# Performance work log

Hardware: AMD Instinct MI355X
Metric: run time of the kernel (lower is better)

Reference implementation:

```python
import jax, jax.numpy as jnp
import numpy as np

N = 100000   # nodes
E = 1200000  # edges
D = 64       # dim == num_features
L = 5        # num_gc_layers
G = 128      # num graphs in batch
BN_EPS = 1e-5
NORM_EPS = 1e-12

def setup_inputs() -> dict:
    key = jax.random.key(0)
    ks = jax.random.split(key, 16)
    s = 0.05
    x = jax.random.normal(ks[0], (N, D), jnp.float32)
    edge_index = jax.random.randint(ks[1], (2, E), 0, N, dtype=jnp.int32)
    batch = jnp.sort(jax.random.randint(ks[2], (N,), 0, G, dtype=jnp.int32))
    # Encoder_support: Linear(D, D)
    Ws = jax.random.normal(ks[3], (D, D), jnp.float32) * s
    bs = jnp.zeros((D,), jnp.float32)
    # GIN MLPs per layer: Linear(D,D) -> ReLU -> Linear(D,D)
    W1 = jax.random.normal(ks[4], (L, D, D), jnp.float32) * s
    b1 = jnp.zeros((L, D), jnp.float32)
    W2 = jax.random.normal(ks[5], (L, D, D), jnp.float32) * s
    b2 = jnp.zeros((L, D), jnp.float32)
    # BatchNorm affine params
    bn_gamma = jnp.ones((L, D), jnp.float32)
    bn_beta = jnp.zeros((L, D), jnp.float32)
    # proj_head: Linear(L*D, L*D) -> ReLU -> Linear(L*D, L*D)
    Wp1 = jax.random.normal(ks[6], (L * D, L * D), jnp.float32) * s
    bp1 = jnp.zeros((L * D,), jnp.float32)
    Wp2 = jax.random.normal(ks[7], (L * D, L * D), jnp.float32) * s
    bp2 = jnp.zeros((L * D,), jnp.float32)
    return {"x": x, "edge_index": edge_index, "batch": batch,
            "Ws": Ws, "bs": bs, "W1": W1, "b1": b1, "W2": W2, "b2": b2,
            "bn_gamma": bn_gamma, "bn_beta": bn_beta,
            "Wp1": Wp1, "bp1": bp1, "Wp2": Wp2, "bp2": bp2}

def _l2norm(v):
    # F.normalize(v, dim=1): v / max(||v||_2, 1e-12)
    n = jnp.sqrt(jnp.sum(v * v, axis=1, keepdims=True))
    return v / jnp.maximum(n, NORM_EPS)

def reference(x, edge_index, batch, Ws, bs, W1, b1, W2, b2,
              bn_gamma, bn_beta, Wp1, bp1, Wp2, bp2):
    src, dst = edge_index[0], edge_index[1]
    h = x @ Ws + bs  # Encoder_support
    xs = []
    for i in range(L):
        # GINConv (eps=0): nn(x + sum_{j->i} x_j)
        agg = jax.ops.segment_sum(h[src], dst, num_segments=N)  # [N, D]
        z = h + agg
        z = jnp.maximum(z @ W1[i] + b1[i], 0.0) @ W2[i] + b2[i]
        z = jnp.maximum(z, 0.0)  # F.relu after conv
        # BatchNorm1d (training-mode batch stats over nodes)
        mean = jnp.mean(z, axis=0)
        var = jnp.var(z, axis=0)
        h = bn_gamma[i] * (z - mean) * jax.lax.rsqrt(var + BN_EPS) + bn_beta[i]
        xs.append(h)
    # global_add_pool per layer, concat along feature dim -> [G, L*D]
    pooled = jnp.concatenate(
        [jax.ops.segment_sum(h_, batch, num_segments=G) for h_ in xs], axis=1)
    y = jnp.maximum(pooled @ Wp1 + bp1, 0.0) @ Wp2 + bp2
    return (_l2norm(y), _l2norm(pooled))
```

## Files before the change

kernel.cpp:

```cpp
#include <hip/hip_runtime.h>
#include <hip/hip_bf16.h>
#include <hip/hip_fp16.h>

constexpr int Nn = 100000;
constexpr int Ee = 1200000;
constexpr int Ll = 5;
constexpr int Gg = 128;
constexpr int PDim = 320;

constexpr int NB    = 98;
constexpr int BCAP  = 16384;
constexpr int CHUNK = 4096;
constexpr int NBLK_A = (Ee + CHUNK - 1) / CHUNK;

typedef short short8 __attribute__((ext_vector_type(8)));
typedef float f32x4 __attribute__((ext_vector_type(4)));

union U4S8 { uint4 u; short8 s; };

__device__ inline ushort f2bf(float f) {
    const uint u = __float_as_uint(f);
    return (ushort)((u + 0x7fffu + ((u >> 16) & 1u)) >> 16);
}
__device__ inline uint pack2(float lo, float hi) {
    return (uint)f2bf(lo) | ((uint)f2bf(hi) << 16);
}
__device__ inline ushort f2h(float f) {
    const __half h = __float2half(f);
    return *(const ushort*)&h;
}
__device__ inline uint pack2h(float lo, float hi) {
    return (uint)f2h(lo) | ((uint)f2h(hi) << 16);
}
__device__ inline float h2f_lo(uint u) {
    const ushort s = (ushort)(u & 0xffffu);
    return __half2float(*(const __half*)&s);
}
__device__ inline float h2f_hi(uint u) {
    const ushort s = (ushort)(u >> 16);
    return __half2float(*(const __half*)&s);
}
__device__ inline void split2(float x0, float x1, uint& hi, uint& lo) {
    const ushort h0 = f2bf(x0), h1 = f2bf(x1);
    hi = (uint)h0 | ((uint)h1 << 16);
    const float r0 = x0 - __uint_as_float((uint)h0 << 16);
    const float r1 = x1 - __uint_as_float((uint)h1 << 16);
    lo = pack2(r0, r1);
}

__device__ inline int lower_bound_i(const int* __restrict__ a, int n, int v)
{
    int lo = 0, hi = n;
    while (lo < hi) {
        const int m = (lo + hi) >> 1;
        if (a[m] < v) lo = m + 1; else hi = m;
    }
    return lo;
}

__global__ void init_csr(const int* __restrict__ batch, int* __restrict__ gCursor,
                         int* __restrict__ cnt, float* __restrict__ sc)
{
    const int t = threadIdx.x;
    if (t < NB) gCursor[t] = t * BCAP;
    {
        const int lo = lower_bound_i(batch, Nn, t);
        const int hi = lower_bound_i(batch, Nn, t + 1);
        cnt[t] = hi - lo;
    }
    if (t < 64) { sc[t] = 1.f; sc[64 + t] = 0.f; }
}

__global__ __launch_bounds__(256) void conv_weights(
    const float* __restrict__ Ws, const float* __restrict__ W1,
    const float* __restrict__ W2, ushort* __restrict__ WThi,
    ushort* __restrict__ WTlo)
{
    const int m = blockIdx.x;
    const float* src = (m == 0) ? Ws
                     : (m <= 5) ? W1 + (size_t)(m - 1) * 4096
                                : W2 + (size_t)(m - 6) * 4096;
    ushort* dh = WThi + (size_t)m * 4096;
    ushort* dl = WTlo + (size_t)m * 4096;
    const int t = threadIdx.x;
    const int col = t & 63;
    const int k0 = (t >> 6) * 16;
    #pragma unroll
    for (int i = 0; i < 16; i++) {
        const int k = k0 + i;
        const float w = src[k * 64 + col];
        const ushort h = f2bf(w);
        dh[col * 64 + k] = h;
        dl[col * 64 + k] = f2bf(w - __uint_as_float((uint)h << 16));
    }
}

__global__ __launch_bounds__(256) void gemm_enc(
    const float* __restrict__ A1,
    const ushort* __restrict__ WThi, const ushort* __restrict__ WTlo,
    const float* __restrict__ bias, ushort* __restrict__ Ys)
{
    const int t = threadIdx.x;
    const int w = t >> 6;
    const int l = t & 63;
    const int lr = l & 15;
    const int lk = l >> 4;

    short8 bHi[4][2], bLo[4][2];
    #pragma unroll
    for (int nt = 0; nt < 4; nt++)
        #pragma unroll
        for (int c = 0; c < 2; c++) {
            const int off = (nt * 16 + lr) * 64 + c * 32 + lk * 8;
            U4S8 uh, ul;
            uh.u = *(const uint4*)(WThi + off);
            ul.u = *(const uint4*)(WTlo + off);
            bHi[nt][c] = uh.s;
            bLo[nt][c] = ul.s;
        }

    const int arow = blockIdx.x * 64 + w * 16 + lr;
    short8 aHi[2], aLo[2];
    if (arow < Nn) {
        #pragma unroll
        for (int c = 0; c < 2; c++) {
            const float* p1 = A1 + (size_t)arow * 64 + c * 32 + lk * 8;
            const float4 v0 = *(const float4*)p1;
            const float4 v1 = *(const float4*)(p1 + 4);
            U4S8 rh, rl;
            uint* ph = (uint*)&rh.u;
            uint* pl = (uint*)&rl.u;
            split2(v0.x, v0.y, ph[0], pl[0]);
            split2(v0.z, v0.w, ph[1], pl[1]);
            split2(v1.x, v1.y, ph[2], pl[2]);
            split2(v1.z, v1.w, ph[3], pl[3]);
            aHi[c] = rh.s;
            aLo[c] = rl.s;
        }
    } else {
        U4S8 z; z.u = make_uint4(0, 0, 0, 0);
        aHi[0] = aHi[1] = z.s;
        aLo[0] = aLo[1] = z.s;
    }

    f32x4 acc[4] = {};
    #pragma unroll
    for (int nt = 0; nt < 4; nt++)
        #pragma unroll
        for (int c = 0; c < 2; c++) {
            acc[nt] = __builtin_amdgcn_mfma_f32_16x16x32_bf16(
                aLo[c], bHi[nt][c], acc[nt], 0, 0, 0);
            acc[nt] = __builtin_amdgcn_mfma_f32_16x16x32_bf16(
                aHi[c], bLo[nt][c], acc[nt], 0, 0, 0);
            acc[nt] = __builtin_amdgcn_mfma_f32_16x16x32_bf16(
                aHi[c], bHi[nt][c], acc[nt], 0, 0, 0);
        }

    #pragma unroll
    for (int nt = 0; nt < 4; nt++) {
        const int ccol = nt * 16 + lr;
        const float bb = bias[ccol];
        #pragma unroll
        for (int j = 0; j < 4; j++) {
            const int crow = blockIdx.x * 64 + w * 16 + lk * 4 + j;
            if (crow < Nn)
                Ys[(size_t)crow * 64 + ccol] = f2h(acc[nt][j] + bb);
        }
    }
}

__global__ __launch_bounds__(256) void fused_mlp(
    const ushort* __restrict__ Us,
    const ushort* __restrict__ WT1hi, const ushort* __restrict__ WT1lo,
    const float* __restrict__ b1v,
    const ushort* __restrict__ WT2hi, const ushort* __restrict__ WT2lo,
    const float* __restrict__ b2v,
    ushort* __restrict__ Zs, float* __restrict__ stats)
{
    const int t = threadIdx.x;
    const int w = t >> 6;
    const int l = t & 63;
    const int lr = l & 15;
    const int lk = l >> 4;

    __shared__ ushort Mh[64][72];
    __shared__ float red[2][4][4][16];

    short8 b1Hi[4][2], b1Lo[4][2];
    #pragma unroll
    for (int nt = 0; nt < 4; nt++)
        #pragma unroll
        for (int c = 0; c < 2; c++) {
            const int off = (nt * 16 + lr) * 64 + c * 32 + lk * 8;
            U4S8 uh, ul;
            uh.u = *(const uint4*)(WT1hi + off);
            ul.u = *(const uint4*)(WT1lo + off);
            b1Hi[nt][c] = uh.s;
            b1Lo[nt][c] = ul.s;
        }

    const int arow = blockIdx.x * 64 + w * 16 + lr;
    short8 aHi[2], aLo[2];
    if (arow < Nn) {
        #pragma unroll
        for (int c = 0; c < 2; c++) {
            const uint4 v = *(const uint4*)(Us + (size_t)arow * 64 + c * 32 + lk * 8);
            U4S8 rh, rl;
            uint* ph = (uint*)&rh.u;
            uint* pl = (uint*)&rl.u;
            split2(h2f_lo(v.x), h2f_hi(v.x), ph[0], pl[0]);
            split2(h2f_lo(v.y), h2f_hi(v.y), ph[1], pl[1]);
            split2(h2f_lo(v.z), h2f_hi(v.z), ph[2], pl[2]);
            split2(h2f_lo(v.w), h2f_hi(v.w), ph[3], pl[3]);
            aHi[c] = rh.s;
            aLo[c] = rl.s;
        }
    } else {
        U4S8 z; z.u = make_uint4(0, 0, 0, 0);
        aHi[0] = aHi[1] = z.s;
        aLo[0] = aLo[1] = z.s;
    }

    f32x4 acc[4] = {};
    #pragma unroll
    for (int nt = 0; nt < 4; nt++)
        #pragma unroll
        for (int c = 0; c < 2; c++) {
            acc[nt] = __builtin_amdgcn_mfma_f32_16x16x32_bf16(
                aLo[c], b1Hi[nt][c], acc[nt], 0, 0, 0);
            acc[nt] = __builtin_amdgcn_mfma_f32_16x16x32_bf16(
                aHi[c], b1Lo[nt][c], acc[nt], 0, 0, 0);
            acc[nt] = __builtin_amdgcn_mfma_f32_16x16x32_bf16(
                aHi[c], b1Hi[nt][c], acc[nt], 0, 0, 0);
        }

    #pragma unroll
    for (int nt = 0; nt < 4; nt++) {
        const int ccol = nt * 16 + lr;
        const float bb = b1v[ccol];
        #pragma unroll
        for (int j = 0; j < 4; j++) {
            const int rloc = w * 16 + lk * 4 + j;
            Mh[rloc][ccol] = f2h(fmaxf(acc[nt][j] + bb, 0.f));
        }
    }
    __syncthreads();

    short8 b2Hi[4][2], b2Lo[4][2];
    #pragma unroll
    for (int nt = 0; nt < 4; nt++)
        #pragma unroll
        for (int c = 0; c < 2; c++) {
            const int off = (nt * 16 + lr) * 64 + c * 32 + lk * 8;
            U4S8 uh, ul;
            uh.u = *(const uint4*)(WT2hi + off);
            ul.u = *(const uint4*)(WT2lo + off);
            b2Hi[nt][c] = uh.s;
            b2Lo[nt][c] = ul.s;
        }

    short8 a2Hi[2], a2Lo[2];
    #pragma unroll
    for (int c = 0; c < 2; c++) {
        const uint4 v = *(const uint4*)&Mh[w * 16 + lr][c * 32 + lk * 8];
        U4S8 rh, rl;
        uint* ph = (uint*)&rh.u;
        uint* pl = (uint*)&rl.u;
        split2(h2f_lo(v.x), h2f_hi(v.x), ph[0], pl[0]);
        split2(h2f_lo(v.y), h2f_hi(v.y), ph[1], pl[1]);
        split2(h2f_lo(v.z), h2f_hi(v.z), ph[2], pl[2]);
        split2(h2f_lo(v.w), h2f_hi(v.w), ph[3], pl[3]);
        a2Hi[c] = rh.s;
        a2Lo[c] = rl.s;
    }

    f32x4 acc2[4] = {};
    #pragma unroll
    for (int nt = 0; nt < 4; nt++)
        #pragma unroll
        for (int c = 0; c < 2; c++) {
            acc2[nt] = __builtin_amdgcn_mfma_f32_16x16x32_bf16(
                a2Lo[c], b2Hi[nt][c], acc2[nt], 0, 0, 0);
            acc2[nt] = __builtin_amdgcn_mfma_f32_16x16x32_bf16(
                a2Hi[c], b2Lo[nt][c], acc2[nt], 0, 0, 0);
            acc2[nt] = __builtin_amdgcn_mfma_f32_16x16x32_bf16(
                a2Hi[c], b2Hi[nt][c], acc2[nt], 0, 0, 0);
        }

    float s[4], s2[4];
    #pragma unroll
    for (int nt = 0; nt < 4; nt++) {
        const int ccol = nt * 16 + lr;
        const float bb = b2v[ccol];
        s[nt] = 0.f; s2[nt] = 0.f;
        #pragma unroll
        for (int j = 0; j < 4; j++) {
            const int crow = blockIdx.x * 64 + w * 16 + lk * 4 + j;
            if (crow < Nn) {
                const float v = fmaxf(acc2[nt][j] + bb, 0.f);
                Zs[(size_t)crow * 64 + ccol] = f2h(v);
                s[nt] += v; s2[nt] += v * v;
            }
        }
    }

    #pragma unroll
    for (int nt = 0; nt < 4; nt++) {
        s[nt]  += __shfl_xor(s[nt], 16);  s[nt]  += __shfl_xor(s[nt], 32);
        s2[nt] += __shfl_xor(s2[nt], 16); s2[nt] += __shfl_xor(s2[nt], 32);
    }
    if (l < 16) {
        #pragma unroll
        for (int nt = 0; nt < 4; nt++) {
            red[0][w][nt][l] = s[nt];
            red[1][w][nt][l] = s2[nt];
        }
    }
    __syncthreads();
    if (t < 64) {
        float ts = 0.f, ts2 = 0.f;
        #pragma unroll
        for (int wv = 0; wv < 4; wv++) {
            ts  += red[0][wv][t >> 4][t & 15];
            ts2 += red[1][wv][t >> 4][t & 15];
        }
        atomicAdd(&stats[t], ts);
        atomicAdd(&stats[64 + t], ts2);
    }
}

__global__ __launch_bounds__(256) void bin_edges(
    const int* __restrict__ ei, int* __restrict__ gCursor,
    uint2* __restrict__ binned)
{
    __shared__ int hist[NB];
    __shared__ int base[NB];
    __shared__ int cur[NB];
    const int t = threadIdx.x;
    const int e0 = blockIdx.x * CHUNK;
    const int eEnd = min(e0 + CHUNK, Ee);
    if (t < NB) hist[t] = 0;
    __syncthreads();
    for (int e = e0 + t; e < eEnd; e += 256)
        atomicAdd(&hist[ei[Ee + e] >> 10], 1);
    __syncthreads();
    if (t < NB) {
        base[t] = atomicAdd(&gCursor[t], hist[t]);
        cur[t] = 0;
    }
    __syncthreads();
    for (int e = e0 + t; e < eEnd; e += 256) {
        const int s = ei[e];
        const int d = ei[Ee + e];
        const int b = d >> 10;
        const int pos = atomicAdd(&cur[b], 1);
        binned[(size_t)base[b] + pos] = make_uint2((uint)d, (uint)s);
    }
}

__global__ __launch_bounds__(128) void scan_buckets(
    const int* __restrict__ gCursor, int* __restrict__ bucketBase)
{
    __shared__ int sh[128];
    const int t = threadIdx.x;
    const int c = (t < NB) ? gCursor[t] - t * BCAP : 0;
    sh[t] = c;
    __syncthreads();
    for (int off = 1; off < 128; off <<= 1) {
        const int u = (t >= off) ? sh[t - off] : 0;
        __syncthreads();
        sh[t] += u;
        __syncthreads();
    }
    bucketBase[t] = sh[t] - c;
}

__global__ __launch_bounds__(256) void build_csr(
    const uint2* __restrict__ binned, const int* __restrict__ gCursor,
    const int* __restrict__ bucketBase, int* __restrict__ rowptr,
    int* __restrict__ colidx)
{
    __shared__ int degS[1024];
    __shared__ int sh[256];
    __shared__ int colStage[BCAP];
    const int b = blockIdx.x;
    const int t = threadIdx.x;
    const int cnt = gCursor[b] - b * BCAP;
    const int base = bucketBase[b];
    const uint2* src = binned + (size_t)b * BCAP;

    for (int i = t; i < 1024; i += 256) degS[i] = 0;
    __syncthreads();
    for (int i = t; i < cnt; i += 256)
        atomicAdd(&degS[src[i].x & 1023], 1);
    __syncthreads();

    const int b4 = t * 4;
    const int v0 = degS[b4], v1 = degS[b4 + 1], v2 = degS[b4 + 2], v3 = degS[b4 + 3];
    const int sSum = v0 + v1 + v2 + v3;
    sh[t] = sSum;
    __syncthreads();
    for (int off = 1; off < 256; off <<= 1) {
        const int u = (t >= off) ? sh[t - off] : 0;
        __syncthreads();
        sh[t] += u;
        __syncthreads();
    }
    const int excl = sh[t] - sSum;
    const int p0 = excl, p1 = excl + v0, p2 = excl + v0 + v1, p3 = excl + v0 + v1 + v2;

    const int grow = b * 1024 + b4;
    if (grow + 3 <= Nn) {
        *(int4*)(rowptr + grow) = make_int4(base + p0, base + p1, base + p2, base + p3);
    } else {
        if (grow + 0 <= Nn) rowptr[grow + 0] = base + p0;
        if (grow + 1 <= Nn) rowptr[grow + 1] = base + p1;
        if (grow + 2 <= Nn) rowptr[grow + 2] = base + p2;
        if (grow + 3 <= Nn) rowptr[grow + 3] = base + p3;
    }

    degS[b4] = p0; degS[b4 + 1] = p1; degS[b4 + 2] = p2; degS[b4 + 3] = p3;
    __syncthreads();
    for (int i = t; i < cnt; i += 256) {
        const uint2 p = src[i];
        const int pos = atomicAdd(&degS[p.x & 1023], 1);
        colStage[pos] = (int)p.y;
    }
    __syncthreads();
    for (int i = t; i < cnt; i += 256) colidx[base + i] = colStage[i];
}

__global__ __launch_bounds__(256) void gather_bn(
    const int* __restrict__ rowptr, const int* __restrict__ col,
    const ushort* __restrict__ zs, const float* __restrict__ sc,
    ushort* __restrict__ us)
{
    __shared__ float scS[128];
    const int t = threadIdx.x;
    if (t < 128) scS[t] = sc[t];
    __syncthreads();

    const int r = blockIdx.x * 32 + (t >> 3);
    const int q = t & 7;
    const int beg = rowptr[r], end = rowptr[r + 1];
    float a[8];
    {
        const uint4 v = *(const uint4*)(zs + (size_t)r * 64 + q * 8);
        a[0] = h2f_lo(v.x); a[1] = h2f_hi(v.x);
        a[2] = h2f_lo(v.y); a[3] = h2f_hi(v.y);
        a[4] = h2f_lo(v.z); a[5] = h2f_hi(v.z);
        a[6] = h2f_lo(v.w); a[7] = h2f_hi(v.w);
    }
    for (int j = beg; j < end; j++) {
        const int s = col[j];
        const uint4 v = *(const uint4*)(zs + (size_t)s * 64 + q * 8);
        a[0] += h2f_lo(v.x); a[1] += h2f_hi(v.x);
        a[2] += h2f_lo(v.y); a[3] += h2f_hi(v.y);
        a[4] += h2f_lo(v.z); a[5] += h2f_hi(v.z);
        a[6] += h2f_lo(v.w); a[7] += h2f_hi(v.w);
    }
    const float dgf = (float)(end - beg + 1);
    float o[8];
    #pragma unroll
    for (int i = 0; i < 8; i++)
        o[i] = fmaf(scS[q * 8 + i], a[i], dgf * scS[64 + q * 8 + i]);
    uint4 p;
    p.x = pack2h(o[0], o[1]); p.y = pack2h(o[2], o[3]);
    p.z = pack2h(o[4], o[5]); p.w = pack2h(o[6], o[7]);
    *(uint4*)(us + (size_t)r * 64 + q * 8) = p;
}

__global__ void bn_finalize(
    float* __restrict__ stats, const float* __restrict__ gamma,
    const float* __restrict__ beta, float* __restrict__ sc,
    float* __restrict__ sc5, int layer)
{
    const int c = threadIdx.x;
    const float mean = stats[c] * (1.0f / Nn);
    const float var = stats[64 + c] * (1.0f / Nn) - mean * mean;
    const float scale = gamma[layer * 64 + c] * rsqrtf(var + 1e-5f);
    const float shift = beta[layer * 64 + c] - mean * scale;
    sc[c] = scale;
    sc[64 + c] = shift;
    sc5[layer * 128 + c] = scale;
    sc5[layer * 128 + 64 + c] = shift;
    stats[c] = 0.f;
    stats[64 + c] = 0.f;
}

__global__ __launch_bounds__(256) void pool_z(
    const ushort* __restrict__ zs, const int* __restrict__ batch,
    float* __restrict__ poolZ)
{
    const int g = blockIdx.x >> 3;
    const int sub = blockIdx.x & 7;
    const int lo = lower_bound_i(batch, Nn, g);
    const int hi = lower_bound_i(batch, Nn, g + 1);
    const int t = threadIdx.x;
    const int cq = t & 15;
    const int rg = (t >> 4) + sub * 16;
    float acc[4] = {};
    for (int row = lo + rg; row < hi; row += 128) {
        const uint2 p = *(const uint2*)(zs + (size_t)row * 64 + cq * 4);
        acc[0] += h2f_lo(p.x); acc[1] += h2f_hi(p.x);
        acc[2] += h2f_lo(p.y); acc[3] += h2f_hi(p.y);
    }
    __shared__ float red[16][16][4];
    #pragma unroll
    for (int i = 0; i < 4; i++) red[t >> 4][cq][i] = acc[i];
    __syncthreads();
    if (t < 64) {
        const int c2 = t >> 2, j = t & 3;
        float s = 0.f;
        #pragma unroll
        for (int r = 0; r < 16; r++) s += red[r][c2][j];
        atomicAdd(&poolZ[g * 64 + c2 * 4 + j], s);
    }
}

__global__ __launch_bounds__(256) void final_pool(
    const float* __restrict__ sc5, const float* __restrict__ poolZ,
    const int* __restrict__ cnt, float* __restrict__ pooled)
{
    const int idx = blockIdx.x * 256 + threadIdx.x;
    const int c = idx & 63;
    const int g = (idx >> 6) & 127;
    const int l = idx >> 13;
    pooled[g * PDim + l * 64 + c] =
        sc5[l * 128 + c] * poolZ[(size_t)l * Gg * 64 + g * 64 + c]
        + (float)cnt[g] * sc5[l * 128 + 64 + c];
}

template<bool RELU>
__global__ __launch_bounds__(256) void proj(
    const float* __restrict__ X, const float* __restrict__ W,
    const float* __restrict__ bias, float* __restrict__ Y)
{
    const int idx = blockIdx.x * 256 + threadIdx.x;
    const int r = idx / PDim;
    const int c = idx - r * PDim;
    float acc = bias[c];
    #pragma unroll 8
    for (int k = 0; k < PDim; k++)
        acc = fmaf(X[r * PDim + k], W[k * PDim + c], acc);
    if constexpr (RELU) acc = fmaxf(acc, 0.f);
    Y[idx] = acc;
}

__global__ __launch_bounds__(64) void l2norm_rows(
    const float* __restrict__ X, float* __restrict__ out)
{
    const int r = blockIdx.x;
    const int l = threadIdx.x;
    float v[5];
    float s = 0.f;
    #pragma unroll
    for (int i = 0; i < 5; i++) {
        v[i] = X[r * PDim + i * 64 + l];
        s += v[i] * v[i];
    }
    #pragma unroll
    for (int off = 32; off > 0; off >>= 1) s += __shfl_down(s, off);
    s = __shfl(s, 0);
    const float d = fmaxf(sqrtf(s), 1e-12f);
    #pragma unroll
    for (int i = 0; i < 5; i++)
        out[r * PDim + i * 64 + l] = v[i] / d;
}

extern "C" void kernel_launch(void* const* d_in, const int* in_sizes, int n_in,
                              void* d_out, int out_size, void* d_ws, size_t ws_size,
                              hipStream_t stream)
{
    const float* x     = (const float*)d_in[0];
    const int*   ei    = (const int*)d_in[1];
    const int*   batch = (const int*)d_in[2];
    const float* Ws    = (const float*)d_in[3];
    const float* bs    = (const float*)d_in[4];
    const float* W1    = (const float*)d_in[5];
    const float* b1    = (const float*)d_in[6];
    const float* W2    = (const float*)d_in[7];
    const float* b2    = (const float*)d_in[8];
    const float* gamma = (const float*)d_in[9];
    const float* beta  = (const float*)d_in[10];
    const float* Wp1   = (const float*)d_in[11];
    const float* bp1   = (const float*)d_in[12];
    const float* Wp2   = (const float*)d_in[13];
    const float* bp2   = (const float*)d_in[14];
    float* out = (float*)d_out;

    ushort* Us = (ushort*)d_ws;
    ushort* Zs = Us + (size_t)Nn * 64;
    ushort* WThi = Zs + (size_t)Nn * 64;
    ushort* WTlo = WThi + 11 * 4096;
    float* pooled = (float*)(WTlo + 11 * 4096);
    float* ytmp   = pooled + (size_t)Gg * PDim;
    float* ypro   = ytmp + (size_t)Gg * PDim;
    float* stats  = ypro + (size_t)Gg * PDim;
    float* sc     = stats + 128;
    float* sc5    = sc + 128;
    float* poolZ  = sc5 + 5 * 128;
    int* cnt    = (int*)(poolZ + 5 * Gg * 64);
    int* rowptr = cnt + 128;
    int* colidx = rowptr + Nn + 1;
    int* gCursor = colidx + Ee;
    int* bucketBase = gCursor + 128;
    size_t woff = (size_t)((bucketBase + 128) - (int*)d_ws);
    woff = (woff + 1) & ~(size_t)1;
    uint2* binned = (uint2*)((int*)d_ws + woff);

    const int gemmGrid = (Nn + 63) / 64;

    hipMemsetAsync(stats, 0, 128 * sizeof(float), stream);
    hipMemsetAsync(poolZ, 0, 5 * Gg * 64 * sizeof(float), stream);

    init_csr<<<1, 128, 0, stream>>>(batch, gCursor, cnt, sc);
    conv_weights<<<11, 256, 0, stream>>>(Ws, W1, W2, WThi, WTlo);

    bin_edges<<<NBLK_A, 256, 0, stream>>>(ei, gCursor, binned);
    scan_buckets<<<1, 128, 0, stream>>>(gCursor, bucketBase);
    build_csr<<<NB, 256, 0, stream>>>(binned, gCursor, bucketBase, rowptr, colidx);

    gemm_enc<<<gemmGrid, 256, 0, stream>>>(x, WThi, WTlo, bs, Zs);

    for (int l = 0; l < Ll; l++) {
        gather_bn<<<Nn / 32, 256, 0, stream>>>(rowptr, colidx, Zs, sc, Us);
        fused_mlp<<<gemmGrid, 256, 0, stream>>>(
            Us,
            WThi + (size_t)(1 + l) * 4096, WTlo + (size_t)(1 + l) * 4096,
            b1 + (size_t)l * 64,
            WThi + (size_t)(6 + l) * 4096, WTlo + (size_t)(6 + l) * 4096,
            b2 + (size_t)l * 64,
            Zs, stats);
        bn_finalize<<<1, 64, 0, stream>>>(stats, gamma, beta, sc, sc5, l);
        pool_z<<<Gg * 8, 256, 0, stream>>>(Zs, batch, poolZ + (size_t)l * Gg * 64);
    }

    final_pool<<<160, 256, 0, stream>>>(sc5, poolZ, cnt, pooled);

    proj<true><<<160, 256, 0, stream>>>(pooled, Wp1, bp1, ytmp);
    proj<false><<<160, 256, 0, stream>>>(ytmp, Wp2, bp2, ypro);

    l2norm_rows<<<Gg, 64, 0, stream>>>(ypro, out);
    l2norm_rows<<<Gg, 64, 0, stream>>>(pooled, out + Gg * PDim);
}
```

Measured before the change: 642.0 us.

## Switch split-precision GEMMs to fp16 MFMA and unroll CSR gather by four

Replaces the bf16 hi/lo three-MFMA emulation with fp16 MFMAs. The weights are split into an fp16 high part and a residual scaled by 2048, and the fp16 activations are fed to the MLP directly without splitting, so two MFMAs per tile replace three and the per-element split arithmetic goes away. The CSR aggregation loop is unrolled by four so that more independent gathers are in flight. Precision now depends on fp16 range for the activations and the scaled residuals, and the unrolled loop reorders the float summation.

```diff
diff --git a/kernel.cpp b/kernel.cpp
--- a/kernel.cpp
+++ b/kernel.cpp
@@ -13,18 +13,11 @@
 constexpr int CHUNK = 4096;
 constexpr int NBLK_A = (Ee + CHUNK - 1) / CHUNK;
 
-typedef short short8 __attribute__((ext_vector_type(8)));
 typedef float f32x4 __attribute__((ext_vector_type(4)));
-
-union U4S8 { uint4 u; short8 s; };
-
-__device__ inline ushort f2bf(float f) {
-    const uint u = __float_as_uint(f);
-    return (ushort)((u + 0x7fffu + ((u >> 16) & 1u)) >> 16);
-}
-__device__ inline uint pack2(float lo, float hi) {
-    return (uint)f2bf(lo) | ((uint)f2bf(hi) << 16);
-}
+typedef _Float16 half8 __attribute__((ext_vector_type(8)));
+
+union U4H8 { uint4 u; half8 h; };
+
 __device__ inline ushort f2h(float f) {
     const __half h = __float2half(f);
     return *(const ushort*)&h;
@@ -39,13 +32,6 @@
 __device__ inline float h2f_hi(uint u) {
     const ushort s = (ushort)(u >> 16);
     return __half2float(*(const __half*)&s);
-}
-__device__ inline void split2(float x0, float x1, uint& hi, uint& lo) {
-    const ushort h0 = f2bf(x0), h1 = f2bf(x1);
-    hi = (uint)h0 | ((uint)h1 << 16);
-    const float r0 = x0 - __uint_as_float((uint)h0 << 16);
-    const float r1 = x1 - __uint_as_float((uint)h1 << 16);
-    lo = pack2(r0, r1);
 }
 
 __device__ inline int lower_bound_i(const int* __restrict__ a, int n, int v)
@@ -89,9 +75,10 @@
     for (int i = 0; i < 16; i++) {
         const int k = k0 + i;
         const float w = src[k * 64 + col];
-        const ushort h = f2bf(w);
+        const ushort h = f2h(w);
         dh[col * 64 + k] = h;
-        dl[col * 64 + k] = f2bf(w - __uint_as_float((uint)h << 16));
+        const float resid = (w - h2f_lo((uint)h)) * 2048.0f;
+        dl[col * 64 + k] = f2h(resid);
     }
 }
 
@@ -106,54 +93,53 @@
     const int lr = l & 15;
     const int lk = l >> 4;
 
-    short8 bHi[4][2], bLo[4][2];
+    half8 bHi[4][2], bLo[4][2];
     #pragma unroll
     for (int nt = 0; nt < 4; nt++)
         #pragma unroll
         for (int c = 0; c < 2; c++) {
             const int off = (nt * 16 + lr) * 64 + c * 32 + lk * 8;
-            U4S8 uh, ul;
+            U4H8 uh, ul;
             uh.u = *(const uint4*)(WThi + off);
             ul.u = *(const uint4*)(WTlo + off);
-            bHi[nt][c] = uh.s;
-            bLo[nt][c] = ul.s;
+            bHi[nt][c] = uh.h;
+            bLo[nt][c] = ul.h;
         }
 
     const int arow = blockIdx.x * 64 + w * 16 + lr;
-    short8 aHi[2], aLo[2];
+    half8 aHi[2], aLo[2];
     if (arow < Nn) {
         #pragma unroll
         for (int c = 0; c < 2; c++) {
             const float* p1 = A1 + (size_t)arow * 64 + c * 32 + lk * 8;
-            const float4 v0 = *(const float4*)p1;
-            const float4 v1 = *(const float4*)(p1 + 4);
-            U4S8 rh, rl;
-            uint* ph = (uint*)&rh.u;
-            uint* pl = (uint*)&rl.u;
-            split2(v0.x, v0.y, ph[0], pl[0]);
-            split2(v0.z, v0.w, ph[1], pl[1]);
-            split2(v1.x, v1.y, ph[2], pl[2]);
-            split2(v1.z, v1.w, ph[3], pl[3]);
-            aHi[c] = rh.s;
-            aLo[c] = rl.s;
+            U4H8 rh, rl;
+            #pragma unroll
+            for (int i = 0; i < 8; i++) {
+                const float xv = p1[i];
+                const _Float16 xh = (_Float16)xv;
+                rh.h[i] = xh;
+                rl.h[i] = (_Float16)((xv - (float)xh) * 2048.0f);
+            }
+            aHi[c] = rh.h;
+            aLo[c] = rl.h;
         }
     } else {
-        U4S8 z; z.u = make_uint4(0, 0, 0, 0);
-        aHi[0] = aHi[1] = z.s;
-        aLo[0] = aLo[1] = z.s;
-    }
-
-    f32x4 acc[4] = {};
+        U4H8 z; z.u = make_uint4(0, 0, 0, 0);
+        aHi[0] = aHi[1] = z.h;
+        aLo[0] = aLo[1] = z.h;
+    }
+
+    f32x4 accH[4] = {}, accL[4] = {};
     #pragma unroll
     for (int nt = 0; nt < 4; nt++)
         #pragma unroll
         for (int c = 0; c < 2; c++) {
-            acc[nt] = __builtin_amdgcn_mfma_f32_16x16x32_bf16(
-                aLo[c], bHi[nt][c], acc[nt], 0, 0, 0);
-            acc[nt] = __builtin_amdgcn_mfma_f32_16x16x32_bf16(
-                aHi[c], bLo[nt][c], acc[nt], 0, 0, 0);
-            acc[nt] = __builtin_amdgcn_mfma_f32_16x16x32_bf16(
-                aHi[c], bHi[nt][c], acc[nt], 0, 0, 0);
+            accH[nt] = __builtin_amdgcn_mfma_f32_16x16x32_f16(
+                aHi[c], bHi[nt][c], accH[nt], 0, 0, 0);
+            accL[nt] = __builtin_amdgcn_mfma_f32_16x16x32_f16(
+                aHi[c], bLo[nt][c], accL[nt], 0, 0, 0);
+            accL[nt] = __builtin_amdgcn_mfma_f32_16x16x32_f16(
+                aLo[c], bHi[nt][c], accL[nt], 0, 0, 0);
         }
 
     #pragma unroll
@@ -164,7 +150,8 @@
         for (int j = 0; j < 4; j++) {
             const int crow = blockIdx.x * 64 + w * 16 + lk * 4 + j;
             if (crow < Nn)
-                Ys[(size_t)crow * 64 + ccol] = f2h(acc[nt][j] + bb);
+                Ys[(size_t)crow * 64 + ccol] =
+                    f2h(fmaf(accL[nt][j], 1.0f / 2048.0f, accH[nt][j]) + bb);
         }
     }
 }
@@ -186,52 +173,41 @@
     __shared__ ushort Mh[64][72];
     __shared__ float red[2][4][4][16];
 
-    short8 b1Hi[4][2], b1Lo[4][2];
+    half8 b1Hi[4][2], b1Lo[4][2];
     #pragma unroll
     for (int nt = 0; nt < 4; nt++)
         #pragma unroll
         for (int c = 0; c < 2; c++) {
             const int off = (nt * 16 + lr) * 64 + c * 32 + lk * 8;
-            U4S8 uh, ul;
+            U4H8 uh, ul;
             uh.u = *(const uint4*)(WT1hi + off);
             ul.u = *(const uint4*)(WT1lo + off);
-            b1Hi[nt][c] = uh.s;
-            b1Lo[nt][c] = ul.s;
+            b1Hi[nt][c] = uh.h;
+            b1Lo[nt][c] = ul.h;
         }
 
     const int arow = blockIdx.x * 64 + w * 16 + lr;
-    short8 aHi[2], aLo[2];
+    half8 aF[2];
     if (arow < Nn) {
+        U4H8 v0, v1;
+        v0.u = *(const uint4*)(Us + (size_t)arow * 64 + lk * 8);
+        v1.u = *(const uint4*)(Us + (size_t)arow * 64 + 32 + lk * 8);
+        aF[0] = v0.h;
+        aF[1] = v1.h;
+    } else {
+        U4H8 z; z.u = make_uint4(0, 0, 0, 0);
+        aF[0] = aF[1] = z.h;
+    }
+
+    f32x4 accH[4] = {}, accL[4] = {};
+    #pragma unroll
+    for (int nt = 0; nt < 4; nt++)
         #pragma unroll
         for (int c = 0; c < 2; c++) {
-            const uint4 v = *(const uint4*)(Us + (size_t)arow * 64 + c * 32 + lk * 8);
-            U4S8 rh, rl;
-            uint* ph = (uint*)&rh.u;
-            uint* pl = (uint*)&rl.u;
-            split2(h2f_lo(v.x), h2f_hi(v.x), ph[0], pl[0]);
-            split2(h2f_lo(v.y), h2f_hi(v.y), ph[1], pl[1]);
-            split2(h2f_lo(v.z), h2f_hi(v.z), ph[2], pl[2]);
-            split2(h2f_lo(v.w), h2f_hi(v.w), ph[3], pl[3]);
-            aHi[c] = rh.s;
-            aLo[c] = rl.s;
-        }
-    } else {
-        U4S8 z; z.u = make_uint4(0, 0, 0, 0);
-        aHi[0] = aHi[1] = z.s;
-        aLo[0] = aLo[1] = z.s;
-    }
-
-    f32x4 acc[4] = {};
-    #pragma unroll
-    for (int nt = 0; nt < 4; nt++)
-        #pragma unroll
-        for (int c = 0; c < 2; c++) {
-            acc[nt] = __builtin_amdgcn_mfma_f32_16x16x32_bf16(
-                aLo[c], b1Hi[nt][c], acc[nt], 0, 0, 0);
-            acc[nt] = __builtin_amdgcn_mfma_f32_16x16x32_bf16(
-                aHi[c], b1Lo[nt][c], acc[nt], 0, 0, 0);
-            acc[nt] = __builtin_amdgcn_mfma_f32_16x16x32_bf16(
-                aHi[c], b1Hi[nt][c], acc[nt], 0, 0, 0);
+            accH[nt] = __builtin_amdgcn_mfma_f32_16x16x32_f16(
+                aF[c], b1Hi[nt][c], accH[nt], 0, 0, 0);
+            accL[nt] = __builtin_amdgcn_mfma_f32_16x16x32_f16(
+                aF[c], b1Lo[nt][c], accL[nt], 0, 0, 0);
         }
 
     #pragma unroll
@@ -241,50 +217,42 @@
         #pragma unroll
         for (int j = 0; j < 4; j++) {
             const int rloc = w * 16 + lk * 4 + j;
-            Mh[rloc][ccol] = f2h(fmaxf(acc[nt][j] + bb, 0.f));
-        }
-    }
-    __syncthreads();
-
-    short8 b2Hi[4][2], b2Lo[4][2];
+            const float m = fmaxf(fmaf(accL[nt][j], 1.0f / 2048.0f, accH[nt][j]) + bb, 0.f);
+            Mh[rloc][ccol] = f2h(m);
+        }
+    }
+    __syncthreads();
+
+    half8 b2Hi[4][2], b2Lo[4][2];
     #pragma unroll
     for (int nt = 0; nt < 4; nt++)
         #pragma unroll
         for (int c = 0; c < 2; c++) {
             const int off = (nt * 16 + lr) * 64 + c * 32 + lk * 8;
-            U4S8 uh, ul;
+            U4H8 uh, ul;
             uh.u = *(const uint4*)(WT2hi + off);
             ul.u = *(const uint4*)(WT2lo + off);
-            b2Hi[nt][c] = uh.s;
-            b2Lo[nt][c] = ul.s;
-        }
-
-    short8 a2Hi[2], a2Lo[2];
+            b2Hi[nt][c] = uh.h;
+            b2Lo[nt][c] = ul.h;
+        }
+
+    half8 a2F[2];
     #pragma unroll
     for (int c = 0; c < 2; c++) {
-        const uint4 v = *(const uint4*)&Mh[w * 16 + lr][c * 32 + lk * 8];
-        U4S8 rh, rl;
-        uint* ph = (uint*)&rh.u;
-        uint* pl = (uint*)&rl.u;
-        split2(h2f_lo(v.x), h2f_hi(v.x), ph[0], pl[0]);
-        split2(h2f_lo(v.y), h2f_hi(v.y), ph[1], pl[1]);
-        split2(h2f_lo(v.z), h2f_hi(v.z), ph[2], pl[2]);
-        split2(h2f_lo(v.w), h2f_hi(v.w), ph[3], pl[3]);
-        a2Hi[c] = rh.s;
-        a2Lo[c] = rl.s;
-    }
-
-    f32x4 acc2[4] = {};
+        U4H8 v;
+        v.u = *(const uint4*)&Mh[w * 16 + lr][c * 32 + lk * 8];
+        a2F[c] = v.h;
+    }
+
+    f32x4 acc2H[4] = {}, acc2L[4] = {};
     #pragma unroll
     for (int nt = 0; nt < 4; nt++)
         #pragma unroll
         for (int c = 0; c < 2; c++) {
-            acc2[nt] = __builtin_amdgcn_mfma_f32_16x16x32_bf16(
-                a2Lo[c], b2Hi[nt][c], acc2[nt], 0, 0, 0);
-            acc2[nt] = __builtin_amdgcn_mfma_f32_16x16x32_bf16(
-                a2Hi[c], b2Lo[nt][c], acc2[nt], 0, 0, 0);
-            acc2[nt] = __builtin_amdgcn_mfma_f32_16x16x32_bf16(
-                a2Hi[c], b2Hi[nt][c], acc2[nt], 0, 0, 0);
+            acc2H[nt] = __builtin_amdgcn_mfma_f32_16x16x32_f16(
+                a2F[c], b2Hi[nt][c], acc2H[nt], 0, 0, 0);
+            acc2L[nt] = __builtin_amdgcn_mfma_f32_16x16x32_f16(
+                a2F[c], b2Lo[nt][c], acc2L[nt], 0, 0, 0);
         }
 
     float s[4], s2[4];
@@ -297,7 +265,7 @@
         for (int j = 0; j < 4; j++) {
             const int crow = blockIdx.x * 64 + w * 16 + lk * 4 + j;
             if (crow < Nn) {
-                const float v = fmaxf(acc2[nt][j] + bb, 0.f);
+                const float v = fmaxf(fmaf(acc2L[nt][j], 1.0f / 2048.0f, acc2H[nt][j]) + bb, 0.f);
                 Zs[(size_t)crow * 64 + ccol] = f2h(v);
                 s[nt] += v; s2[nt] += v * v;
             }
@@ -451,7 +419,24 @@
         a[4] = h2f_lo(v.z); a[5] = h2f_hi(v.z);
         a[6] = h2f_lo(v.w); a[7] = h2f_hi(v.w);
     }
-    for (int j = beg; j < end; j++) {
+    int j = beg;
+    const int end4 = beg + ((end - beg) & ~3);
+    for (; j < end4; j += 4) {
+        const int s0 = col[j], s1 = col[j + 1], s2 = col[j + 2], s3 = col[j + 3];
+        const uint4 v0 = *(const uint4*)(zs + (size_t)s0 * 64 + q * 8);
+        const uint4 v1 = *(const uint4*)(zs + (size_t)s1 * 64 + q * 8);
+        const uint4 v2 = *(const uint4*)(zs + (size_t)s2 * 64 + q * 8);
+        const uint4 v3 = *(const uint4*)(zs + (size_t)s3 * 64 + q * 8);
+        a[0] += h2f_lo(v0.x) + h2f_lo(v1.x) + h2f_lo(v2.x) + h2f_lo(v3.x);
+        a[1] += h2f_hi(v0.x) + h2f_hi(v1.x) + h2f_hi(v2.x) + h2f_hi(v3.x);
+        a[2] += h2f_lo(v0.y) + h2f_lo(v1.y) + h2f_lo(v2.y) + h2f_lo(v3.y);
+        a[3] += h2f_hi(v0.y) + h2f_hi(v1.y) + h2f_hi(v2.y) + h2f_hi(v3.y);
+        a[4] += h2f_lo(v0.z) + h2f_lo(v1.z) + h2f_lo(v2.z) + h2f_lo(v3.z);
+        a[5] += h2f_hi(v0.z) + h2f_hi(v1.z) + h2f_hi(v2.z) + h2f_hi(v3.z);
+        a[6] += h2f_lo(v0.w) + h2f_lo(v1.w) + h2f_lo(v2.w) + h2f_lo(v3.w);
+        a[7] += h2f_hi(v0.w) + h2f_hi(v1.w) + h2f_hi(v2.w) + h2f_hi(v3.w);
+    }
+    for (; j < end; j++) {
         const int s = col[j];
         const uint4 v = *(const uint4*)(zs + (size_t)s * 64 + q * 8);
         a[0] += h2f_lo(v.x); a[1] += h2f_hi(v.x);
```

Measured after the change: 632.3 us. No clear change (-1.5%).
